# Kernel optimization log

Measured on AMD Instinct MI355X. Metric: run time of the kernel, lower is better.

## Reference

```python
import jax, jax.numpy as jnp
import numpy as np

N = 100000   # nodes
E = 1600000  # edges
IN = 768     # in_dim
H = 128      # hidden_dim
G = 64       # graphs per batch


def setup_inputs() -> dict:
    key = jax.random.key(0)
    ks = jax.random.split(key, 9)
    x = jax.random.normal(ks[0], (N, IN), jnp.float32)
    edge_index = jax.random.randint(ks[1], (2, E), 0, N, dtype=jnp.int64)
    batch = jnp.sort(jax.random.randint(ks[2], (N,), 0, G, dtype=jnp.int64))
    W1 = jax.random.normal(ks[3], (IN, H), jnp.float32) / np.float32(np.sqrt(IN))
    b1 = jax.random.normal(ks[4], (H,), jnp.float32) * 0.01
    W2 = jax.random.normal(ks[5], (H, H), jnp.float32) / np.float32(np.sqrt(H))
    b2 = jax.random.normal(ks[6], (H,), jnp.float32) * 0.01
    Wh = jax.random.normal(ks[7], (H, 2), jnp.float32) / np.float32(np.sqrt(H))
    bh = jax.random.normal(ks[8], (2,), jnp.float32) * 0.01
    return dict(x=x, edge_index=edge_index, batch=batch, W1=W1, b1=b1,
                W2=W2, b2=b2, Wh=Wh, bh=bh, num_graphs=G)


def gcn_conv(x, src, dst, W, b, n):
    # PyG GCNConv default: add self-loops (already in src/dst), symmetric norm.
    deg = jax.ops.segment_sum(jnp.ones_like(dst, x.dtype), dst, num_segments=n)
    dis = jnp.where(deg > 0, jax.lax.rsqrt(deg), jnp.zeros_like(deg))
    h = x @ W                                   # [n, out]
    norm = (dis[src] * dis[dst])[:, None]       # [E+n, 1]
    out = jax.ops.segment_sum(h[src] * norm, dst, num_segments=n)
    return out + b


def reference(x, edge_index, batch, W1, b1, W2, b2, Wh, bh, num_graphs):
    n = x.shape[0]
    loop = jnp.arange(n, dtype=edge_index.dtype)
    src = jnp.concatenate([edge_index[0], loop])
    dst = jnp.concatenate([edge_index[1], loop])
    h = jax.nn.relu(gcn_conv(x, src, dst, W1, b1, n))   # dropout = eval identity
    h = jax.nn.relu(gcn_conv(h, src, dst, W2, b2, n))
    summed = jax.ops.segment_sum(h, batch, num_segments=num_graphs)
    counts = jax.ops.segment_sum(jnp.ones((n, 1), h.dtype), batch, num_segments=num_graphs)
    emb = summed / jnp.maximum(counts, 1.0)             # global_mean_pool
    return emb @ Wh + bh
```

## Files before the change

kernel.cpp:

```cpp
#include <hip/hip_runtime.h>
#include <hip/hip_bf16.h>

static constexpr int N_NODES  = 100000;
static constexpr int N_EDGES  = 1600000;
static constexpr int DIM_IN   = 768;
static constexpr int DIM_H    = 128;
static constexpr int N_GRAPHS = 64;
static constexpr int NB_SCAN  = (N_NODES + 255) / 256;

typedef __attribute__((ext_vector_type(8))) short short8;
typedef __attribute__((ext_vector_type(4))) float f32x4;

__device__ __forceinline__ ushort f2bf(float f) {
    union { float f; uint u; } v; v.f = f;
    uint r = v.u + 0x7fffu + ((v.u >> 16) & 1u);
    return (ushort)(r >> 16);
}
__device__ __forceinline__ float bf2f(ushort u) {
    union { uint u; float f; } v; v.u = ((uint)u) << 16;
    return v.f;
}

__global__ void k_indeg(const int* __restrict__ edst, int* __restrict__ indeg) {
    int e = blockIdx.x * 256 + threadIdx.x;
    if (e < N_EDGES) atomicAdd(&indeg[edst[e]], 1);
}

__global__ void k_scan1(const int* __restrict__ indeg, int* __restrict__ rp,
                        int* __restrict__ bsum, float* __restrict__ dis) {
    __shared__ int s[256];
    int t = threadIdx.x;
    int i = blockIdx.x * 256 + t;
    int v = (i < N_NODES) ? indeg[i] : 0;
    s[t] = v;
    __syncthreads();
    for (int off = 1; off < 256; off <<= 1) {
        int x = (t >= off) ? s[t - off] : 0;
        __syncthreads();
        s[t] += x;
        __syncthreads();
    }
    if (i < N_NODES) {
        rp[i] = s[t] - v;
        dis[i] = rsqrtf((float)v + 1.0f);
    }
    if (t == 255) bsum[blockIdx.x] = s[255];
}

__global__ void k_scan2(int* __restrict__ bsum, const int* __restrict__ batch,
                        int* __restrict__ gstart) {
    __shared__ int s[512];
    int t = threadIdx.x;
    int v = (t < NB_SCAN) ? bsum[t] : 0;
    s[t] = v;
    __syncthreads();
    for (int off = 1; off < 512; off <<= 1) {
        int x = (t >= off) ? s[t - off] : 0;
        __syncthreads();
        s[t] += x;
        __syncthreads();
    }
    if (t < NB_SCAN) bsum[t] = s[t] - v;
    if (t <= N_GRAPHS) {
        int lo = 0, hi = N_NODES;
        while (lo < hi) {
            int mid = (lo + hi) >> 1;
            if (batch[mid] < t) lo = mid + 1; else hi = mid;
        }
        gstart[t] = lo;
    }
}

__global__ void k_scatter(const int* __restrict__ esrc, const int* __restrict__ edst,
                          const int* __restrict__ rp, const int* __restrict__ bsum,
                          const float* __restrict__ dis,
                          int* __restrict__ cursor, uint2* __restrict__ csrw) {
    int e = blockIdx.x * 256 + threadIdx.x;
    if (e >= N_EDGES) return;
    int d = edst[e];
    int sv = esrc[e];
    int pos = atomicAdd(&cursor[d], 1);
    uint2 val;
    val.x = (uint)sv;
    val.y = __float_as_uint(dis[sv]);
    csrw[rp[d] + bsum[d >> 8] + pos] = val;
}

__global__ void k_convW(const float* __restrict__ W1, const float* __restrict__ W2,
                        ushort* __restrict__ W1th, ushort* __restrict__ W1tl,
                        ushort* __restrict__ W2th, ushort* __restrict__ W2tl) {
    int i = blockIdx.x * 256 + threadIdx.x;
    const int total1 = DIM_IN * DIM_H;
    if (i < total1) {
        int k = i >> 7, n = i & 127;
        float w = W1[i];
        ushort h = f2bf(w);
        ushort lo = f2bf(w - bf2f(h));
        W1th[(size_t)n * DIM_IN + k] = h;
        W1tl[(size_t)n * DIM_IN + k] = lo;
    } else {
        int j = i - total1;
        if (j < DIM_H * DIM_H) {
            int k = j >> 7, n = j & 127;
            float w = W2[j];
            ushort h = f2bf(w);
            ushort lo = f2bf(w - bf2f(h));
            W2th[(size_t)n * DIM_H + k] = h;
            W2tl[(size_t)n * DIM_H + k] = lo;
        }
    }
}

#define LDSTR 40

template<int K, bool AFP32>
__global__ __launch_bounds__(256) void k_gemm_mfma(const void* __restrict__ Av,
                                                   const ushort* __restrict__ Wth,
                                                   const ushort* __restrict__ Wtl,
                                                   ushort* __restrict__ C,
                                                   int nrows) {
    __shared__ ushort As[128 * LDSTR];
    __shared__ ushort Bh[128 * LDSTR];
    __shared__ ushort Bl[128 * LDSTR];

    const int t = threadIdx.x;
    const int row0 = blockIdx.x * 128;
    const int srow = t >> 1;
    const int skoff = (t & 1) * 16;
    const int l = t & 63;
    const int wv = t >> 6;
    const int wm = wv >> 1, wn = wv & 1;
    const int lr = l & 15;
    const int lk = (l >> 4) * 8;

    f32x4 acc[4][4];
    const f32x4 zero = {0.f, 0.f, 0.f, 0.f};
    #pragma unroll
    for (int m = 0; m < 4; ++m)
        #pragma unroll
        for (int n = 0; n < 4; ++n) acc[m][n] = zero;

    for (int k0 = 0; k0 < K; k0 += 32) {
        {
            uint p[8];
            if (AFP32) {
                float f[16];
                if (row0 + srow < nrows) {
                    const float4* Ap = (const float4*)((const float*)Av +
                        (size_t)(row0 + srow) * K + k0 + skoff);
                    *(float4*)&f[0]  = Ap[0];
                    *(float4*)&f[4]  = Ap[1];
                    *(float4*)&f[8]  = Ap[2];
                    *(float4*)&f[12] = Ap[3];
                } else {
                    #pragma unroll
                    for (int i = 0; i < 16; ++i) f[i] = 0.f;
                }
                #pragma unroll
                for (int i = 0; i < 8; ++i)
                    p[i] = (uint)f2bf(f[2 * i]) | ((uint)f2bf(f[2 * i + 1]) << 16);
            } else {
                uint4 q0 = {0, 0, 0, 0}, q1 = {0, 0, 0, 0};
                if (row0 + srow < nrows) {
                    const uint4* Ap = (const uint4*)((const ushort*)Av +
                        (size_t)(row0 + srow) * K + k0 + skoff);
                    q0 = Ap[0]; q1 = Ap[1];
                }
                p[0] = q0.x; p[1] = q0.y; p[2] = q0.z; p[3] = q0.w;
                p[4] = q1.x; p[5] = q1.y; p[6] = q1.z; p[7] = q1.w;
            }
            uint4 w0 = {p[0], p[1], p[2], p[3]};
            uint4 w1 = {p[4], p[5], p[6], p[7]};
            *(uint4*)&As[srow * LDSTR + skoff]     = w0;
            *(uint4*)&As[srow * LDSTR + skoff + 8] = w1;
        }
        {
            const uint4* Wp = (const uint4*)(Wth + (size_t)srow * K + k0 + skoff);
            *(uint4*)&Bh[srow * LDSTR + skoff]     = Wp[0];
            *(uint4*)&Bh[srow * LDSTR + skoff + 8] = Wp[1];
            const uint4* Wq = (const uint4*)(Wtl + (size_t)srow * K + k0 + skoff);
            *(uint4*)&Bl[srow * LDSTR + skoff]     = Wq[0];
            *(uint4*)&Bl[srow * LDSTR + skoff + 8] = Wq[1];
        }
        __syncthreads();

        short8 a[4], bh[4], bl[4];
        #pragma unroll
        for (int m = 0; m < 4; ++m)
            a[m] = *(const short8*)&As[(wm * 64 + m * 16 + lr) * LDSTR + lk];
        #pragma unroll
        for (int n = 0; n < 4; ++n) {
            bh[n] = *(const short8*)&Bh[(wn * 64 + n * 16 + lr) * LDSTR + lk];
            bl[n] = *(const short8*)&Bl[(wn * 64 + n * 16 + lr) * LDSTR + lk];
        }
        #pragma unroll
        for (int m = 0; m < 4; ++m)
            #pragma unroll
            for (int n = 0; n < 4; ++n) {
                acc[m][n] = __builtin_amdgcn_mfma_f32_16x16x32_bf16(a[m], bh[n], acc[m][n], 0, 0, 0);
                acc[m][n] = __builtin_amdgcn_mfma_f32_16x16x32_bf16(a[m], bl[n], acc[m][n], 0, 0, 0);
            }
        __syncthreads();
    }

    #pragma unroll
    for (int m = 0; m < 4; ++m) {
        #pragma unroll
        for (int n = 0; n < 4; ++n) {
            int col = wn * 64 + n * 16 + lr;
            #pragma unroll
            for (int j = 0; j < 4; ++j) {
                int row = row0 + wm * 64 + m * 16 + (l >> 4) * 4 + j;
                if (row < nrows)
                    C[(size_t)row * DIM_H + col] = f2bf(acc[m][n][j]);
            }
        }
    }
}

__device__ __forceinline__ void acc8(uint4 u, float w, float* a) {
    a[0] += bf2f((ushort)(u.x & 0xffff)) * w;
    a[1] += bf2f((ushort)(u.x >> 16))    * w;
    a[2] += bf2f((ushort)(u.y & 0xffff)) * w;
    a[3] += bf2f((ushort)(u.y >> 16))    * w;
    a[4] += bf2f((ushort)(u.z & 0xffff)) * w;
    a[5] += bf2f((ushort)(u.z >> 16))    * w;
    a[6] += bf2f((ushort)(u.w & 0xffff)) * w;
    a[7] += bf2f((ushort)(u.w >> 16))    * w;
}

__global__ __launch_bounds__(256) void k_agg(const ushort* __restrict__ hin,
                                             const uint2* __restrict__ csrw,
                                             const int* __restrict__ rp,
                                             const int* __restrict__ bsum,
                                             const int* __restrict__ indeg,
                                             const float* __restrict__ dis,
                                             const float* __restrict__ bias,
                                             ushort* __restrict__ hout) {
    int node = (blockIdx.x * 256 + threadIdx.x) >> 6;
    int lane = threadIdx.x & 63;
    if (node >= N_NODES) return;
    int q  = lane >> 4;
    int cl = lane & 15;
    float di = dis[node];
    int beg = rp[node] + bsum[node >> 8];
    int cnt = indeg[node];

    float a[8] = {0.f, 0.f, 0.f, 0.f, 0.f, 0.f, 0.f, 0.f};

    {
        uint s; float w;
        if (q == 0)             { s = (uint)node; w = di * di; }
        else if (q - 1 < cnt)   { uint2 p = csrw[beg + q - 1]; s = p.x; w = __uint_as_float(p.y) * di; }
        else                    { s = (uint)node; w = 0.f; }
        uint4 u = ((const uint4*)(hin + (size_t)s * DIM_H))[cl];
        acc8(u, w, a);
    }
    const uint2* cp = csrw + beg + 3;
    int m = cnt - 3;
    int i = 0;
    for (; i + 8 <= m; i += 8) {
        uint2 p0 = cp[i + q];
        uint2 p1 = cp[i + 4 + q];
        float w0 = __uint_as_float(p0.y) * di;
        float w1 = __uint_as_float(p1.y) * di;
        uint4 u0 = ((const uint4*)(hin + (size_t)p0.x * DIM_H))[cl];
        uint4 u1 = ((const uint4*)(hin + (size_t)p1.x * DIM_H))[cl];
        acc8(u0, w0, a);
        acc8(u1, w1, a);
    }
    for (; i < m; i += 4) {
        int idx = i + q;
        uint s; float w;
        if (idx < m) { uint2 p = cp[idx]; s = p.x; w = __uint_as_float(p.y) * di; }
        else         { s = (uint)node;    w = 0.f; }
        uint4 u = ((const uint4*)(hin + (size_t)s * DIM_H))[cl];
        acc8(u, w, a);
    }

    #pragma unroll
    for (int j = 0; j < 8; ++j) {
        a[j] += __shfl_xor(a[j], 16);
        a[j] += __shfl_xor(a[j], 32);
    }

    if (q == 0) {
        float4 b0 = ((const float4*)bias)[cl * 2];
        float4 b1 = ((const float4*)bias)[cl * 2 + 1];
        float o0 = fmaxf(a[0] + b0.x, 0.f), o1 = fmaxf(a[1] + b0.y, 0.f);
        float o2 = fmaxf(a[2] + b0.z, 0.f), o3 = fmaxf(a[3] + b0.w, 0.f);
        float o4 = fmaxf(a[4] + b1.x, 0.f), o5 = fmaxf(a[5] + b1.y, 0.f);
        float o6 = fmaxf(a[6] + b1.z, 0.f), o7 = fmaxf(a[7] + b1.w, 0.f);
        uint4 o;
        o.x = (uint)f2bf(o0) | ((uint)f2bf(o1) << 16);
        o.y = (uint)f2bf(o2) | ((uint)f2bf(o3) << 16);
        o.z = (uint)f2bf(o4) | ((uint)f2bf(o5) << 16);
        o.w = (uint)f2bf(o6) | ((uint)f2bf(o7) << 16);
        ((uint4*)(hout + (size_t)node * DIM_H))[cl] = o;
    }
}

#define PSPLIT 8
__global__ __launch_bounds__(256) void k_pool(const ushort* __restrict__ h,
                                              const int* __restrict__ gstart,
                                              float* __restrict__ pooled2) {
    int g  = blockIdx.x >> 3;
    int sp = blockIdx.x & 7;
    int r0 = gstart[g], r1 = gstart[g + 1];
    int count = r1 - r0;
    int chunk = (count + PSPLIT - 1) / PSPLIT;
    int aS = r0 + sp * chunk;
    int bE = min(aS + chunk, r1);
    int c  = threadIdx.x & 63;
    int rr = threadIdx.x >> 6;
    float s0 = 0.f, s1 = 0.f;
    for (int r = aS + rr; r < bE; r += 4) {
        uint u = ((const uint*)(h + (size_t)r * DIM_H))[c];
        s0 += bf2f((ushort)(u & 0xffff));
        s1 += bf2f((ushort)(u >> 16));
    }
    __shared__ float sm0[4][64], sm1[4][64];
    sm0[rr][c] = s0; sm1[rr][c] = s1;
    __syncthreads();
    if (rr == 0) {
        float v0 = sm0[0][c] + sm0[1][c] + sm0[2][c] + sm0[3][c];
        float v1 = sm1[0][c] + sm1[1][c] + sm1[2][c] + sm1[3][c];
        float* dst = pooled2 + (size_t)(g * PSPLIT + sp) * DIM_H;
        dst[2 * c]     = v0;
        dst[2 * c + 1] = v1;
    }
}

__global__ __launch_bounds__(128) void k_head(const float* __restrict__ pooled2,
                                              const int* __restrict__ gstart,
                                              const float* __restrict__ Wh,
                                              const float* __restrict__ bh,
                                              float* __restrict__ out) {
    int g = blockIdx.x;
    int c = threadIdx.x;
    float s = 0.f;
    #pragma unroll
    for (int sp = 0; sp < PSPLIT; ++sp)
        s += pooled2[(size_t)(g * PSPLIT + sp) * DIM_H + c];
    float cntg = (float)(gstart[g + 1] - gstart[g]);
    float e = s / fmaxf(cntg, 1.0f);
    __shared__ float s0[128], s1[128];
    s0[c] = e * Wh[c * 2 + 0];
    s1[c] = e * Wh[c * 2 + 1];
    __syncthreads();
    for (int off = 64; off > 0; off >>= 1) {
        if (c < off) { s0[c] += s0[c + off]; s1[c] += s1[c + off]; }
        __syncthreads();
    }
    if (c == 0) {
        out[g * 2 + 0] = s0[0] + bh[0];
        out[g * 2 + 1] = s1[0] + bh[1];
    }
}

extern "C" void kernel_launch(void* const* d_in, const int* in_sizes, int n_in,
                              void* d_out, int out_size, void* d_ws, size_t ws_size,
                              hipStream_t stream) {
    const float* x    = (const float*)d_in[0];
    const int*   esrc = (const int*)d_in[1];
    const int*   edst = esrc + N_EDGES;
    const int*   batch= (const int*)d_in[2];
    const float* W1   = (const float*)d_in[3];
    const float* b1   = (const float*)d_in[4];
    const float* W2   = (const float*)d_in[5];
    const float* b2   = (const float*)d_in[6];
    const float* Wh   = (const float*)d_in[7];
    const float* bh   = (const float*)d_in[8];
    float* out = (float*)d_out;

    char* ws = (char*)d_ws;
    size_t off = 0;
    auto alloc = [&](size_t bytes) {
        void* p = ws + off;
        off += (bytes + 255) & ~(size_t)255;
        return p;
    };
    ushort* bufZ   = (ushort*)alloc((size_t)N_NODES * DIM_H * 2);
    ushort* bufH   = (ushort*)alloc((size_t)N_NODES * DIM_H * 2);
    float*  dis    = (float*)alloc((size_t)N_NODES * 4);
    int*    deg2   = (int*)  alloc((size_t)2 * N_NODES * 4);
    int*    indeg  = deg2;
    int*    cursor = deg2 + N_NODES;
    int*    rp     = (int*)  alloc((size_t)N_NODES * 4);
    uint2*  csrw   = (uint2*)alloc((size_t)N_EDGES * 8);
    int*    bsum   = (int*)  alloc(512 * 4);
    float*  pooled2= (float*)alloc((size_t)N_GRAPHS * PSPLIT * DIM_H * 4);
    int*    gstart = (int*)  alloc((N_GRAPHS + 1) * 4);
    ushort* W1th   = (ushort*)alloc((size_t)DIM_IN * DIM_H * 2);
    ushort* W1tl   = (ushort*)alloc((size_t)DIM_IN * DIM_H * 2);
    ushort* W2th   = (ushort*)alloc((size_t)DIM_H * DIM_H * 2);
    ushort* W2tl   = (ushort*)alloc((size_t)DIM_H * DIM_H * 2);

    hipMemsetAsync(deg2, 0, (size_t)2 * N_NODES * 4, stream);

    int convblocks = (DIM_IN * DIM_H + DIM_H * DIM_H + 255) / 256;
    k_convW  <<<convblocks, 256, 0, stream>>>(W1, W2, W1th, W1tl, W2th, W2tl);

    k_indeg  <<<(N_EDGES + 255) / 256, 256, 0, stream>>>(edst, indeg);
    k_scan1  <<<NB_SCAN, 256, 0, stream>>>(indeg, rp, bsum, dis);
    k_scan2  <<<1, 512, 0, stream>>>(bsum, batch, gstart);
    k_scatter<<<(N_EDGES + 255) / 256, 256, 0, stream>>>(esrc, edst, rp, bsum, dis, cursor, csrw);

    int gblocks = (N_NODES + 127) / 128;
    k_gemm_mfma<DIM_IN, true ><<<gblocks, 256, 0, stream>>>(x,    W1th, W1tl, bufZ, N_NODES);
    k_agg<<<(N_NODES + 3) / 4, 256, 0, stream>>>(bufZ, csrw, rp, bsum, indeg, dis, b1, bufH);
    k_gemm_mfma<DIM_H,  false><<<gblocks, 256, 0, stream>>>(bufH, W2th, W2tl, bufZ, N_NODES);
    k_agg<<<(N_NODES + 3) / 4, 256, 0, stream>>>(bufZ, csrw, rp, bsum, indeg, dis, b2, bufH);

    k_pool<<<N_GRAPHS * PSPLIT, 256, 0, stream>>>(bufH, gstart, pooled2);
    k_head<<<N_GRAPHS, 128, 0, stream>>>(pooled2, gstart, Wh, bh, out);
}
```

Before: 453.4 us.

## Switch GEMMs and intermediates to fp16, drop split-bf16 weights, fuse small kernels

Replaces the hi/lo split bf16 weight scheme, which needed two MFMAs per tile, with single fp16 weights and fp16 MFMA, halving matrix work and B-tile shared memory traffic. Intermediate activations become fp16 instead of bf16, keeping accuracy without the extra low-part product. Weight conversion is merged into the in-degree kernel, and pooling plus the head are fused into one kernel with fewer blocks. This risks fp16 overflow or precision loss on activations, and the pooling now uses only 64 blocks, which lowers parallelism for that step.

```diff
diff --git a/kernel.cpp b/kernel.cpp
--- a/kernel.cpp
+++ b/kernel.cpp
@@ -1,5 +1,6 @@
 #include <hip/hip_runtime.h>
 #include <hip/hip_bf16.h>
+#include <hip/hip_fp16.h>
 
 static constexpr int N_NODES  = 100000;
 static constexpr int N_EDGES  = 1600000;
@@ -8,22 +9,23 @@
 static constexpr int N_GRAPHS = 64;
 static constexpr int NB_SCAN  = (N_NODES + 255) / 256;
 
-typedef __attribute__((ext_vector_type(8))) short short8;
+typedef __attribute__((ext_vector_type(8))) _Float16 half8;
 typedef __attribute__((ext_vector_type(4))) float f32x4;
 
-__device__ __forceinline__ ushort f2bf(float f) {
-    union { float f; uint u; } v; v.f = f;
-    uint r = v.u + 0x7fffu + ((v.u >> 16) & 1u);
-    return (ushort)(r >> 16);
-}
-__device__ __forceinline__ float bf2f(ushort u) {
-    union { uint u; float f; } v; v.u = ((uint)u) << 16;
-    return v.f;
-}
-
-__global__ void k_indeg(const int* __restrict__ edst, int* __restrict__ indeg) {
-    int e = blockIdx.x * 256 + threadIdx.x;
-    if (e < N_EDGES) atomicAdd(&indeg[edst[e]], 1);
+__global__ void k_pre(const float* __restrict__ W1, const float* __restrict__ W2,
+                      _Float16* __restrict__ W1t, _Float16* __restrict__ W2t,
+                      const int* __restrict__ edst, int* __restrict__ indeg) {
+    int i = blockIdx.x * 256 + threadIdx.x;
+    if (i < N_EDGES) atomicAdd(&indeg[edst[i]], 1);
+    const int total1 = DIM_IN * DIM_H;
+    if (i < total1) {
+        int k = i >> 7, n = i & 127;
+        W1t[(size_t)n * DIM_IN + k] = (_Float16)W1[i];
+    } else if (i < total1 + DIM_H * DIM_H) {
+        int j = i - total1;
+        int k = j >> 7, n = j & 127;
+        W2t[(size_t)n * DIM_H + k] = (_Float16)W2[j];
+    }
 }
 
 __global__ void k_scan1(const int* __restrict__ indeg, int* __restrict__ rp,
@@ -86,42 +88,15 @@
     csrw[rp[d] + bsum[d >> 8] + pos] = val;
 }
 
-__global__ void k_convW(const float* __restrict__ W1, const float* __restrict__ W2,
-                        ushort* __restrict__ W1th, ushort* __restrict__ W1tl,
-                        ushort* __restrict__ W2th, ushort* __restrict__ W2tl) {
-    int i = blockIdx.x * 256 + threadIdx.x;
-    const int total1 = DIM_IN * DIM_H;
-    if (i < total1) {
-        int k = i >> 7, n = i & 127;
-        float w = W1[i];
-        ushort h = f2bf(w);
-        ushort lo = f2bf(w - bf2f(h));
-        W1th[(size_t)n * DIM_IN + k] = h;
-        W1tl[(size_t)n * DIM_IN + k] = lo;
-    } else {
-        int j = i - total1;
-        if (j < DIM_H * DIM_H) {
-            int k = j >> 7, n = j & 127;
-            float w = W2[j];
-            ushort h = f2bf(w);
-            ushort lo = f2bf(w - bf2f(h));
-            W2th[(size_t)n * DIM_H + k] = h;
-            W2tl[(size_t)n * DIM_H + k] = lo;
-        }
-    }
-}
-
 #define LDSTR 40
 
 template<int K, bool AFP32>
 __global__ __launch_bounds__(256) void k_gemm_mfma(const void* __restrict__ Av,
-                                                   const ushort* __restrict__ Wth,
-                                                   const ushort* __restrict__ Wtl,
-                                                   ushort* __restrict__ C,
+                                                   const _Float16* __restrict__ Wt,
+                                                   _Float16* __restrict__ C,
                                                    int nrows) {
     __shared__ ushort As[128 * LDSTR];
-    __shared__ ushort Bh[128 * LDSTR];
-    __shared__ ushort Bl[128 * LDSTR];
+    __shared__ ushort Bs[128 * LDSTR];
 
     const int t = threadIdx.x;
     const int row0 = blockIdx.x * 128;
@@ -141,65 +116,53 @@
         for (int n = 0; n < 4; ++n) acc[m][n] = zero;
 
     for (int k0 = 0; k0 < K; k0 += 32) {
+        if (AFP32) {
+            union { _Float16 h[16]; uint4 q[2]; } cv;
+            float f[16];
+            if (row0 + srow < nrows) {
+                const float4* Ap = (const float4*)((const float*)Av +
+                    (size_t)(row0 + srow) * K + k0 + skoff);
+                *(float4*)&f[0]  = Ap[0];
+                *(float4*)&f[4]  = Ap[1];
+                *(float4*)&f[8]  = Ap[2];
+                *(float4*)&f[12] = Ap[3];
+            } else {
+                #pragma unroll
+                for (int i = 0; i < 16; ++i) f[i] = 0.f;
+            }
+            #pragma unroll
+            for (int i = 0; i < 16; ++i) cv.h[i] = (_Float16)f[i];
+            *(uint4*)&As[srow * LDSTR + skoff]     = cv.q[0];
+            *(uint4*)&As[srow * LDSTR + skoff + 8] = cv.q[1];
+        } else {
+            uint4 q0 = {0, 0, 0, 0}, q1 = {0, 0, 0, 0};
+            if (row0 + srow < nrows) {
+                const uint4* Ap = (const uint4*)((const _Float16*)Av +
+                    (size_t)(row0 + srow) * K + k0 + skoff);
+                q0 = Ap[0]; q1 = Ap[1];
+            }
+            *(uint4*)&As[srow * LDSTR + skoff]     = q0;
+            *(uint4*)&As[srow * LDSTR + skoff + 8] = q1;
+        }
         {
-            uint p[8];
-            if (AFP32) {
-                float f[16];
-                if (row0 + srow < nrows) {
-                    const float4* Ap = (const float4*)((const float*)Av +
-                        (size_t)(row0 + srow) * K + k0 + skoff);
-                    *(float4*)&f[0]  = Ap[0];
-                    *(float4*)&f[4]  = Ap[1];
-                    *(float4*)&f[8]  = Ap[2];
-                    *(float4*)&f[12] = Ap[3];
-                } else {
-                    #pragma unroll
-                    for (int i = 0; i < 16; ++i) f[i] = 0.f;
-                }
-                #pragma unroll
-                for (int i = 0; i < 8; ++i)
-                    p[i] = (uint)f2bf(f[2 * i]) | ((uint)f2bf(f[2 * i + 1]) << 16);
-            } else {
-                uint4 q0 = {0, 0, 0, 0}, q1 = {0, 0, 0, 0};
-                if (row0 + srow < nrows) {
-                    const uint4* Ap = (const uint4*)((const ushort*)Av +
-                        (size_t)(row0 + srow) * K + k0 + skoff);
-                    q0 = Ap[0]; q1 = Ap[1];
-                }
-                p[0] = q0.x; p[1] = q0.y; p[2] = q0.z; p[3] = q0.w;
-                p[4] = q1.x; p[5] = q1.y; p[6] = q1.z; p[7] = q1.w;
-            }
-            uint4 w0 = {p[0], p[1], p[2], p[3]};
-            uint4 w1 = {p[4], p[5], p[6], p[7]};
-            *(uint4*)&As[srow * LDSTR + skoff]     = w0;
-            *(uint4*)&As[srow * LDSTR + skoff + 8] = w1;
-        }
-        {
-            const uint4* Wp = (const uint4*)(Wth + (size_t)srow * K + k0 + skoff);
-            *(uint4*)&Bh[srow * LDSTR + skoff]     = Wp[0];
-            *(uint4*)&Bh[srow * LDSTR + skoff + 8] = Wp[1];
-            const uint4* Wq = (const uint4*)(Wtl + (size_t)srow * K + k0 + skoff);
-            *(uint4*)&Bl[srow * LDSTR + skoff]     = Wq[0];
-            *(uint4*)&Bl[srow * LDSTR + skoff + 8] = Wq[1];
-        }
-        __syncthreads();
-
-        short8 a[4], bh[4], bl[4];
+            const uint4* Wp = (const uint4*)(Wt + (size_t)srow * K + k0 + skoff);
+            *(uint4*)&Bs[srow * LDSTR + skoff]     = Wp[0];
+            *(uint4*)&Bs[srow * LDSTR + skoff + 8] = Wp[1];
+        }
+        __syncthreads();
+
+        half8 a[4], b[4];
         #pragma unroll
         for (int m = 0; m < 4; ++m)
-            a[m] = *(const short8*)&As[(wm * 64 + m * 16 + lr) * LDSTR + lk];
-        #pragma unroll
-        for (int n = 0; n < 4; ++n) {
-            bh[n] = *(const short8*)&Bh[(wn * 64 + n * 16 + lr) * LDSTR + lk];
-            bl[n] = *(const short8*)&Bl[(wn * 64 + n * 16 + lr) * LDSTR + lk];
-        }
+            a[m] = *(const half8*)&As[(wm * 64 + m * 16 + lr) * LDSTR + lk];
+        #pragma unroll
+        for (int n = 0; n < 4; ++n)
+            b[n] = *(const half8*)&Bs[(wn * 64 + n * 16 + lr) * LDSTR + lk];
         #pragma unroll
         for (int m = 0; m < 4; ++m)
             #pragma unroll
-            for (int n = 0; n < 4; ++n) {
-                acc[m][n] = __builtin_amdgcn_mfma_f32_16x16x32_bf16(a[m], bh[n], acc[m][n], 0, 0, 0);
-                acc[m][n] = __builtin_amdgcn_mfma_f32_16x16x32_bf16(a[m], bl[n], acc[m][n], 0, 0, 0);
-            }
+            for (int n = 0; n < 4; ++n)
+                acc[m][n] = __builtin_amdgcn_mfma_f32_16x16x32_f16(a[m], b[n], acc[m][n], 0, 0, 0);
         __syncthreads();
     }
 
@@ -212,31 +175,31 @@
             for (int j = 0; j < 4; ++j) {
                 int row = row0 + wm * 64 + m * 16 + (l >> 4) * 4 + j;
                 if (row < nrows)
-                    C[(size_t)row * DIM_H + col] = f2bf(acc[m][n][j]);
+                    C[(size_t)row * DIM_H + col] = (_Float16)acc[m][n][j];
             }
         }
     }
 }
 
 __device__ __forceinline__ void acc8(uint4 u, float w, float* a) {
-    a[0] += bf2f((ushort)(u.x & 0xffff)) * w;
-    a[1] += bf2f((ushort)(u.x >> 16))    * w;
-    a[2] += bf2f((ushort)(u.y & 0xffff)) * w;
-    a[3] += bf2f((ushort)(u.y >> 16))    * w;
-    a[4] += bf2f((ushort)(u.z & 0xffff)) * w;
-    a[5] += bf2f((ushort)(u.z >> 16))    * w;
-    a[6] += bf2f((ushort)(u.w & 0xffff)) * w;
-    a[7] += bf2f((ushort)(u.w >> 16))    * w;
-}
-
-__global__ __launch_bounds__(256) void k_agg(const ushort* __restrict__ hin,
+    __half2 h0 = *(__half2*)&u.x;
+    __half2 h1 = *(__half2*)&u.y;
+    __half2 h2 = *(__half2*)&u.z;
+    __half2 h3 = *(__half2*)&u.w;
+    a[0] += __low2float(h0) * w; a[1] += __high2float(h0) * w;
+    a[2] += __low2float(h1) * w; a[3] += __high2float(h1) * w;
+    a[4] += __low2float(h2) * w; a[5] += __high2float(h2) * w;
+    a[6] += __low2float(h3) * w; a[7] += __high2float(h3) * w;
+}
+
+__global__ __launch_bounds__(256) void k_agg(const _Float16* __restrict__ hin,
                                              const uint2* __restrict__ csrw,
                                              const int* __restrict__ rp,
                                              const int* __restrict__ bsum,
                                              const int* __restrict__ indeg,
                                              const float* __restrict__ dis,
                                              const float* __restrict__ bias,
-                                             ushort* __restrict__ hout) {
+                                             _Float16* __restrict__ hout) {
     int node = (blockIdx.x * 256 + threadIdx.x) >> 6;
     int lane = threadIdx.x & 63;
     if (node >= N_NODES) return;
@@ -287,74 +250,51 @@
     if (q == 0) {
         float4 b0 = ((const float4*)bias)[cl * 2];
         float4 b1 = ((const float4*)bias)[cl * 2 + 1];
-        float o0 = fmaxf(a[0] + b0.x, 0.f), o1 = fmaxf(a[1] + b0.y, 0.f);
-        float o2 = fmaxf(a[2] + b0.z, 0.f), o3 = fmaxf(a[3] + b0.w, 0.f);
-        float o4 = fmaxf(a[4] + b1.x, 0.f), o5 = fmaxf(a[5] + b1.y, 0.f);
-        float o6 = fmaxf(a[6] + b1.z, 0.f), o7 = fmaxf(a[7] + b1.w, 0.f);
+        __half2 h0 = __floats2half2_rn(fmaxf(a[0] + b0.x, 0.f), fmaxf(a[1] + b0.y, 0.f));
+        __half2 h1 = __floats2half2_rn(fmaxf(a[2] + b0.z, 0.f), fmaxf(a[3] + b0.w, 0.f));
+        __half2 h2 = __floats2half2_rn(fmaxf(a[4] + b1.x, 0.f), fmaxf(a[5] + b1.y, 0.f));
+        __half2 h3 = __floats2half2_rn(fmaxf(a[6] + b1.z, 0.f), fmaxf(a[7] + b1.w, 0.f));
         uint4 o;
-        o.x = (uint)f2bf(o0) | ((uint)f2bf(o1) << 16);
-        o.y = (uint)f2bf(o2) | ((uint)f2bf(o3) << 16);
-        o.z = (uint)f2bf(o4) | ((uint)f2bf(o5) << 16);
-        o.w = (uint)f2bf(o6) | ((uint)f2bf(o7) << 16);
+        o.x = *(uint*)&h0; o.y = *(uint*)&h1; o.z = *(uint*)&h2; o.w = *(uint*)&h3;
         ((uint4*)(hout + (size_t)node * DIM_H))[cl] = o;
     }
 }
 
-#define PSPLIT 8
-__global__ __launch_bounds__(256) void k_pool(const ushort* __restrict__ h,
-                                              const int* __restrict__ gstart,
-                                              float* __restrict__ pooled2) {
-    int g  = blockIdx.x >> 3;
-    int sp = blockIdx.x & 7;
+__global__ __launch_bounds__(256) void k_poolhead(const _Float16* __restrict__ h,
+                                                  const int* __restrict__ gstart,
+                                                  const float* __restrict__ Wh,
+                                                  const float* __restrict__ bh,
+                                                  float* __restrict__ out) {
+    int g = blockIdx.x;
     int r0 = gstart[g], r1 = gstart[g + 1];
-    int count = r1 - r0;
-    int chunk = (count + PSPLIT - 1) / PSPLIT;
-    int aS = r0 + sp * chunk;
-    int bE = min(aS + chunk, r1);
     int c  = threadIdx.x & 63;
     int rr = threadIdx.x >> 6;
     float s0 = 0.f, s1 = 0.f;
-    for (int r = aS + rr; r < bE; r += 4) {
+    for (int r = r0 + rr; r < r1; r += 4) {
         uint u = ((const uint*)(h + (size_t)r * DIM_H))[c];
-        s0 += bf2f((ushort)(u & 0xffff));
-        s1 += bf2f((ushort)(u >> 16));
+        __half2 hh = *(__half2*)&u;
+        s0 += __low2float(hh);
+        s1 += __high2float(hh);
     }
     __shared__ float sm0[4][64], sm1[4][64];
     sm0[rr][c] = s0; sm1[rr][c] = s1;
     __syncthreads();
-    if (rr == 0) {
+    if (threadIdx.x < 64) {
         float v0 = sm0[0][c] + sm0[1][c] + sm0[2][c] + sm0[3][c];
         float v1 = sm1[0][c] + sm1[1][c] + sm1[2][c] + sm1[3][c];
-        float* dst = pooled2 + (size_t)(g * PSPLIT + sp) * DIM_H;
-        dst[2 * c]     = v0;
-        dst[2 * c + 1] = v1;
-    }
-}
-
-__global__ __launch_bounds__(128) void k_head(const float* __restrict__ pooled2,
-                                              const int* __restrict__ gstart,
-                                              const float* __restrict__ Wh,
-                                              const float* __restrict__ bh,
-                                              float* __restrict__ out) {
-    int g = blockIdx.x;
-    int c = threadIdx.x;
-    float s = 0.f;
-    #pragma unroll
-    for (int sp = 0; sp < PSPLIT; ++sp)
-        s += pooled2[(size_t)(g * PSPLIT + sp) * DIM_H + c];
-    float cntg = (float)(gstart[g + 1] - gstart[g]);
-    float e = s / fmaxf(cntg, 1.0f);
-    __shared__ float s0[128], s1[128];
-    s0[c] = e * Wh[c * 2 + 0];
-    s1[c] = e * Wh[c * 2 + 1];
-    __syncthreads();
-    for (int off = 64; off > 0; off >>= 1) {
-        if (c < off) { s0[c] += s0[c + off]; s1[c] += s1[c + off]; }
-        __syncthreads();
-    }
-    if (c == 0) {
-        out[g * 2 + 0] = s0[0] + bh[0];
-        out[g * 2 + 1] = s1[0] + bh[1];
+        float inv = 1.f / fmaxf((float)(r1 - r0), 1.f);
+        float e0 = v0 * inv, e1 = v1 * inv;
+        float g0 = e0 * Wh[(2 * c) * 2 + 0] + e1 * Wh[(2 * c + 1) * 2 + 0];
+        float g1 = e0 * Wh[(2 * c) * 2 + 1] + e1 * Wh[(2 * c + 1) * 2 + 1];
+        #pragma unroll
+        for (int off = 32; off > 0; off >>= 1) {
+            g0 += __shfl_down(g0, off);
+            g1 += __shfl_down(g1, off);
+        }
+        if (c == 0) {
+            out[g * 2 + 0] = g0 + bh[0];
+            out[g * 2 + 1] = g1 + bh[1];
+        }
     }
 }
 
@@ -380,38 +320,31 @@
         off += (bytes + 255) & ~(size_t)255;
         return p;
     };
-    ushort* bufZ   = (ushort*)alloc((size_t)N_NODES * DIM_H * 2);
-    ushort* bufH   = (ushort*)alloc((size_t)N_NODES * DIM_H * 2);
-    float*  dis    = (float*)alloc((size_t)N_NODES * 4);
-    int*    deg2   = (int*)  alloc((size_t)2 * N_NODES * 4);
-    int*    indeg  = deg2;
-    int*    cursor = deg2 + N_NODES;
-    int*    rp     = (int*)  alloc((size_t)N_NODES * 4);
-    uint2*  csrw   = (uint2*)alloc((size_t)N_EDGES * 8);
-    int*    bsum   = (int*)  alloc(512 * 4);
-    float*  pooled2= (float*)alloc((size_t)N_GRAPHS * PSPLIT * DIM_H * 4);
-    int*    gstart = (int*)  alloc((N_GRAPHS + 1) * 4);
-    ushort* W1th   = (ushort*)alloc((size_t)DIM_IN * DIM_H * 2);
-    ushort* W1tl   = (ushort*)alloc((size_t)DIM_IN * DIM_H * 2);
-    ushort* W2th   = (ushort*)alloc((size_t)DIM_H * DIM_H * 2);
-    ushort* W2tl   = (ushort*)alloc((size_t)DIM_H * DIM_H * 2);
+    _Float16* bufZ  = (_Float16*)alloc((size_t)N_NODES * DIM_H * 2);
+    _Float16* bufH  = (_Float16*)alloc((size_t)N_NODES * DIM_H * 2);
+    float*    dis   = (float*)alloc((size_t)N_NODES * 4);
+    int*      deg2  = (int*)  alloc((size_t)2 * N_NODES * 4);
+    int*      indeg = deg2;
+    int*      cursor= deg2 + N_NODES;
+    int*      rp    = (int*)  alloc((size_t)N_NODES * 4);
+    uint2*    csrw  = (uint2*)alloc((size_t)N_EDGES * 8);
+    int*      bsum  = (int*)  alloc(512 * 4);
+    int*      gstart= (int*)  alloc((N_GRAPHS + 1) * 4);
+    _Float16* W1t   = (_Float16*)alloc((size_t)DIM_IN * DIM_H * 2);
+    _Float16* W2t   = (_Float16*)alloc((size_t)DIM_H * DIM_H * 2);
 
     hipMemsetAsync(deg2, 0, (size_t)2 * N_NODES * 4, stream);
 
-    int convblocks = (DIM_IN * DIM_H + DIM_H * DIM_H + 255) / 256;
-    k_convW  <<<convblocks, 256, 0, stream>>>(W1, W2, W1th, W1tl, W2th, W2tl);
-
-    k_indeg  <<<(N_EDGES + 255) / 256, 256, 0, stream>>>(edst, indeg);
+    k_pre    <<<(N_EDGES + 255) / 256, 256, 0, stream>>>(W1, W2, W1t, W2t, edst, indeg);
     k_scan1  <<<NB_SCAN, 256, 0, stream>>>(indeg, rp, bsum, dis);
     k_scan2  <<<1, 512, 0, stream>>>(bsum, batch, gstart);
     k_scatter<<<(N_EDGES + 255) / 256, 256, 0, stream>>>(esrc, edst, rp, bsum, dis, cursor, csrw);
 
     int gblocks = (N_NODES + 127) / 128;
-    k_gemm_mfma<DIM_IN, true ><<<gblocks, 256, 0, stream>>>(x,    W1th, W1tl, bufZ, N_NODES);
+    k_gemm_mfma<DIM_IN, true ><<<gblocks, 256, 0, stream>>>(x,    W1t, bufZ, N_NODES);
     k_agg<<<(N_NODES + 3) / 4, 256, 0, stream>>>(bufZ, csrw, rp, bsum, indeg, dis, b1, bufH);
-    k_gemm_mfma<DIM_H,  false><<<gblocks, 256, 0, stream>>>(bufH, W2th, W2tl, bufZ, N_NODES);
+    k_gemm_mfma<DIM_H,  false><<<gblocks, 256, 0, stream>>>(bufH, W2t, bufZ, N_NODES);
     k_agg<<<(N_NODES + 3) / 4, 256, 0, stream>>>(bufZ, csrw, rp, bsum, indeg, dis, b2, bufH);
 
-    k_pool<<<N_GRAPHS * PSPLIT, 256, 0, stream>>>(bufH, gstart, pooled2);
-    k_head<<<N_GRAPHS, 128, 0, stream>>>(pooled2, gstart, Wh, bh, out);
-}
+    k_poolhead<<<N_GRAPHS, 256, 0, stream>>>(bufH, gstart, Wh, bh, out);
+}
```

New measurement: 533.9 us. 17.8% more time.
